# Kernel tuning notes

Hardware: AMD Instinct MI355X
Metric: run time of the kernel (lower is better)

## Reference

```python
import jax, jax.numpy as jnp
import numpy as np

B, S, D = 1024, 48, 256   # graphs, nodes-per-graph, embedding dim (= input_dim)
GDIM = 512                # graph_dim
N = B * S                 # total nodes
E = 4 * N                 # directed edges (avg degree ~4, molecular graphs)
W_SCALE = 0.05


def setup_inputs() -> dict:
    key = jax.random.key(0)
    ks = jax.random.split(key, 8)
    return {
        "sub2gene_out": jax.random.normal(ks[0], (B, S, D), jnp.float32),
        "edge_index": jax.random.randint(ks[1], (2, E), 0, N, dtype=jnp.int64),
        # conv1: in_channels = 2*D (concat of x and laplacian-smoothed x)
        "W_l1": jax.random.normal(ks[2], (GDIM, 2 * D), jnp.float32) * W_SCALE,
        "W_r1": jax.random.normal(ks[3], (GDIM, 2 * D), jnp.float32) * W_SCALE,
        "b1": jnp.zeros((GDIM,), jnp.float32),
        # conv2: graph_dim -> graph_dim
        "W_l2": jax.random.normal(ks[4], (GDIM, GDIM), jnp.float32) * W_SCALE,
        "W_r2": jax.random.normal(ks[5], (GDIM, GDIM), jnp.float32) * W_SCALE,
        "b2": jnp.zeros((GDIM,), jnp.float32),
    }


def sage_conv(x, src, dst, W_l, W_r, b, n):
    """PyG SAGEConv (mean aggregation, root_weight=True):
    out_i = W_l @ mean_{j in N(i)} x_j + W_r @ x_i + b, messages flow src->dst."""
    msg = x[src]                                            # [E, F] gather
    agg = jax.ops.segment_sum(msg, dst, num_segments=n)     # [N, F]
    cnt = jax.ops.segment_sum(jnp.ones((src.shape[0],), x.dtype), dst, num_segments=n)
    mean = agg / jnp.maximum(cnt, 1.0)[:, None]
    return mean @ W_l.T + x @ W_r.T + b


def reference(sub2gene_out, edge_index, W_l1, W_r1, b1, W_l2, W_r2, b2):
    b_, s_, d_ = sub2gene_out.shape
    n = b_ * s_
    x = sub2gene_out.reshape(n, d_)                         # cat of per-graph node features
    row, col = edge_index[0], edge_index[1]

    # sym-normalized Laplacian L = I - D^{-1/2} A D^{-1/2}; lap_x = L @ x
    ones_e = jnp.ones((row.shape[0],), x.dtype)
    deg = jax.ops.segment_sum(ones_e, row, num_segments=n)
    dinv = jnp.where(deg > 0, 1.0, 0.0) / jnp.sqrt(jnp.maximum(deg, 1.0))
    w = -(dinv[row] * dinv[col])                            # off-diagonal -A_norm
    lap_x = x + jax.ops.segment_sum(w[:, None] * x[col], row, num_segments=n)

    x_comb = jnp.concatenate([x, lap_x], axis=-1)           # [N, 2D]
    h = jax.nn.gelu(sage_conv(x_comb, row, col, W_l1, W_r1, b1, n), approximate=False)
    h = sage_conv(h, row, col, W_l2, W_r2, b2, n)           # [N, GDIM]

    # global_mean_pool: every graph has exactly s_ nodes
    batch = jnp.repeat(jnp.arange(b_), s_)
    pooled = jax.ops.segment_sum(h, batch, num_segments=b_) / jnp.asarray(s_, h.dtype)
    return pooled                                           # [B, GDIM]
```

## Files before the change

kernel.cpp:

```cpp
#include <hip/hip_runtime.h>
#include <math.h>

typedef unsigned short u16;
typedef __attribute__((ext_vector_type(8))) short bf16x8;
typedef __attribute__((ext_vector_type(4))) float f32x4;

#define NB 1024
#define NS 48
#define ND 256
#define NN (NB*NS)
#define NE (4*NN)
#define GD 512
#define KK 1024

__device__ __forceinline__ void gld16(const void* g, void* l) {
  __builtin_amdgcn_global_load_lds(
      (const __attribute__((address_space(1))) void*)(void*)g,
      (__attribute__((address_space(3))) void*)l, 16, 0, 0);
}

__device__ __forceinline__ float bf2f(u16 h) {
  unsigned u = ((unsigned)h) << 16; float f; __builtin_memcpy(&f, &u, 4); return f;
}
__device__ __forceinline__ u16 f2bf(float f) {
  unsigned u; __builtin_memcpy(&u, &f, 4);
  u += 0x7fffu + ((u >> 16) & 1u);
  return (u16)(u >> 16);
}
__device__ __forceinline__ void unpack8(uint4 v, float* f) {
  f[0]=bf2f((u16)(v.x & 0xffff)); f[1]=bf2f((u16)(v.x >> 16));
  f[2]=bf2f((u16)(v.y & 0xffff)); f[3]=bf2f((u16)(v.y >> 16));
  f[4]=bf2f((u16)(v.z & 0xffff)); f[5]=bf2f((u16)(v.z >> 16));
  f[6]=bf2f((u16)(v.w & 0xffff)); f[7]=bf2f((u16)(v.w >> 16));
}
__device__ __forceinline__ uint4 pack8(const float* f) {
  uint4 v;
  v.x = (unsigned)f2bf(f[0]) | ((unsigned)f2bf(f[1]) << 16);
  v.y = (unsigned)f2bf(f[2]) | ((unsigned)f2bf(f[3]) << 16);
  v.z = (unsigned)f2bf(f[4]) | ((unsigned)f2bf(f[5]) << 16);
  v.w = (unsigned)f2bf(f[6]) | ((unsigned)f2bf(f[7]) << 16);
  return v;
}


__global__ void k_hist(const int* __restrict__ ei, int* __restrict__ deg, int* __restrict__ cnt) {
  int e = blockIdx.x * 256 + threadIdx.x;
  if (e < NE) {
    atomicAdd(&deg[ei[e]], 1);
    atomicAdd(&cnt[ei[NE + e]], 1);
  }
}

__global__ void k_exscan2(const int* __restrict__ deg, const int* __restrict__ cnt,
                          int* __restrict__ rowOff, int* __restrict__ colOff,
                          float* __restrict__ dinv) {
  const int t = threadIdx.x;
  const int base = t * 48;
  if (blockIdx.x == 2) {
    for (int i = 0; i < 48; ++i) {
      int d = deg[base + i];
      dinv[base + i] = (d > 0) ? rsqrtf((float)d) : 0.0f;
    }
    return;
  }
  __shared__ int sums[1024];
  const int* in = blockIdx.x ? cnt : deg;
  int* out = blockIdx.x ? colOff : rowOff;
  int s = 0;
  for (int i = 0; i < 48; ++i) s += in[base + i];
  sums[t] = s;
  __syncthreads();
  for (int off = 1; off < 1024; off <<= 1) {
    int v = (t >= off) ? sums[t - off] : 0;
    __syncthreads();
    sums[t] += v;
    __syncthreads();
  }
  int run = (t == 0) ? 0 : sums[t - 1];
  for (int i = 0; i < 48; ++i) { int v = in[base + i]; out[base + i] = run; run += v; }
  if (t == 1023) out[NN] = run;
}

__global__ void k_fill(const int* __restrict__ ei,
                       const int* __restrict__ rowOff, const int* __restrict__ colOff,
                       int* __restrict__ rowFill, int* __restrict__ colFill,
                       int* __restrict__ rowCol, int* __restrict__ colSrc) {
  int e = blockIdx.x * 256 + threadIdx.x;
  if (e < NE) {
    int r = ei[e], c = ei[NE + e];
    int pr = atomicAdd(&rowFill[r], 1);
    rowCol[rowOff[r] + pr] = c;
    int pc = atomicAdd(&colFill[c], 1);
    colSrc[colOff[c] + pc] = r;
  }
}

__global__ void k_wx(const float* __restrict__ Wr1, const float* __restrict__ Wl1,
                     const float* __restrict__ Wr2, const float* __restrict__ Wl2,
                     u16* __restrict__ W1c, u16* __restrict__ W2c,
                     const float* __restrict__ x, u16* __restrict__ xb) {
  const int b = blockIdx.x;
  if (b < 1024) {
    const float* Wr = (b < 512) ? Wr1 : Wr2;
    const float* Wl = (b < 512) ? Wl1 : Wl2;
    u16* Wc = (b < 512) ? W1c : W2c;
    int i = ((b & 511) * 256 + threadIdx.x) * 4;
    int n = i >> 10, k = i & 1023;
    const float* src = (k < 512) ? (Wr + n * 512 + k) : (Wl + n * 512 + (k - 512));
    float4 v = *(const float4*)src;
    ushort4 h; h.x = f2bf(v.x); h.y = f2bf(v.y); h.z = f2bf(v.z); h.w = f2bf(v.w);
    *(ushort4*)(Wc + i) = h;
  } else {
    int i = ((b - 1024) * 256 + threadIdx.x) * 8;
    float4 v0 = *(const float4*)(x + i);
    float4 v1 = *(const float4*)(x + i + 4);
    float f[8] = {v0.x, v0.y, v0.z, v0.w, v1.x, v1.y, v1.z, v1.w};
    *(uint4*)(xb + i) = pack8(f);
  }
}

__global__ void k_lap(const u16* __restrict__ xb, const int* __restrict__ rowOff,
                      const int* __restrict__ rowCol, const float* __restrict__ dinv,
                      u16* __restrict__ xcomb) {
  const int gid = blockIdx.x * 256 + threadIdx.x;
  const int wid = gid >> 6, lane = gid & 63;
  const int node = wid * 2 + (lane >> 5);
  const int f0 = (lane & 31) * 8;
  float xi[8]; unpack8(*(const uint4*)(xb + (size_t)node * ND + f0), xi);
  float a[8] = {};
  const int s0 = rowOff[node], s1 = rowOff[node + 1];
  for (int p = s0; p < s1; p += 4) {
    const int q1 = (p + 1 < s1) ? p + 1 : s1 - 1;
    const int q2 = (p + 2 < s1) ? p + 2 : s1 - 1;
    const int q3 = (p + 3 < s1) ? p + 3 : s1 - 1;
    const int c0 = rowCol[p], c1 = rowCol[q1], c2 = rowCol[q2], c3 = rowCol[q3];
    const float w0 = dinv[c0];
    const float w1 = (p + 1 < s1) ? dinv[c1] : 0.f;
    const float w2 = (p + 2 < s1) ? dinv[c2] : 0.f;
    const float w3 = (p + 3 < s1) ? dinv[c3] : 0.f;
    float g0[8], g1[8], g2[8], g3[8];
    unpack8(*(const uint4*)(xb + (size_t)c0 * ND + f0), g0);
    unpack8(*(const uint4*)(xb + (size_t)c1 * ND + f0), g1);
    unpack8(*(const uint4*)(xb + (size_t)c2 * ND + f0), g2);
    unpack8(*(const uint4*)(xb + (size_t)c3 * ND + f0), g3);
    #pragma unroll
    for (int j = 0; j < 8; ++j) a[j] += w0 * g0[j] + w1 * g1[j] + w2 * g2[j] + w3 * g3[j];
  }
  const float di = dinv[node];
  u16* dst = xcomb + (size_t)node * KK + f0;
  *(uint4*)dst = pack8(xi);
  float l[8];
  #pragma unroll
  for (int j = 0; j < 8; ++j) l[j] = xi[j] - di * a[j];
  *(uint4*)(dst + ND) = pack8(l);
}

__global__ void k_aggx(u16* __restrict__ xcomb, const int* __restrict__ colOff,
                       const int* __restrict__ colSrc) {
  const int gid = blockIdx.x * 256 + threadIdx.x;
  const int node = gid >> 6, lane = gid & 63;
  const int f0 = lane * 8;
  float acc[8] = {};
  const int s0 = colOff[node], s1 = colOff[node + 1];
  for (int p = s0; p < s1; p += 4) {
    const int q1 = (p + 1 < s1) ? p + 1 : s1 - 1;
    const int q2 = (p + 2 < s1) ? p + 2 : s1 - 1;
    const int q3 = (p + 3 < s1) ? p + 3 : s1 - 1;
    const int c0 = colSrc[p], c1 = colSrc[q1], c2 = colSrc[q2], c3 = colSrc[q3];
    const float w1 = (p + 1 < s1) ? 1.f : 0.f;
    const float w2 = (p + 2 < s1) ? 1.f : 0.f;
    const float w3 = (p + 3 < s1) ? 1.f : 0.f;
    float g0[8], g1[8], g2[8], g3[8];
    unpack8(*(const uint4*)(xcomb + (size_t)c0 * KK + f0), g0);
    unpack8(*(const uint4*)(xcomb + (size_t)c1 * KK + f0), g1);
    unpack8(*(const uint4*)(xcomb + (size_t)c2 * KK + f0), g2);
    unpack8(*(const uint4*)(xcomb + (size_t)c3 * KK + f0), g3);
    #pragma unroll
    for (int j = 0; j < 8; ++j) acc[j] += g0[j] + w1 * g1[j] + w2 * g2[j] + w3 * g3[j];
  }
  const float inv = (s1 > s0) ? 1.0f / (float)(s1 - s0) : 1.0f;
  float res[8];
  #pragma unroll
  for (int j = 0; j < 8; ++j) res[j] = acc[j] * inv;
  *(uint4*)(xcomb + (size_t)node * KK + 512 + f0) = pack8(res);
}

template <int MODE>
__global__ __launch_bounds__(256) void k_gemm(const u16* __restrict__ A,
                                              const u16* __restrict__ Bw,
                                              const float* __restrict__ bias,
                                              void* __restrict__ OutP) {
  __shared__ u16 As[2][128 * 32];
  __shared__ u16 Bs[2][128 * 32];
  const int tid = threadIdx.x;
  const int w = tid >> 6, lane = tid & 63;
  const int wr = w >> 1, wc = w & 1;

  const int cpx = gridDim.x >> 3;
  const int o = blockIdx.x;
  const int swz = (o & 7) * cpx + (o >> 3);
  const int bx = swz >> 2;
  const int by = swz & 3;

  const int c0 = w * 2, c1 = c0 + 1;
  const int lrow = lane >> 2;
  const int lcol = ((lane & 3) ^ ((lane >> 3) & 3)) * 8;
  const u16* Ag0 = A  + (size_t)(bx * 128 + c0 * 16 + lrow) * KK + lcol;
  const u16* Ag1 = A  + (size_t)(bx * 128 + c1 * 16 + lrow) * KK + lcol;
  const u16* Bg0 = Bw + (size_t)(by * 128 + c0 * 16 + lrow) * KK + lcol;
  const u16* Bg1 = Bw + (size_t)(by * 128 + c1 * 16 + lrow) * KK + lcol;

  const int kslot = ((lane >> 4) ^ ((lane >> 1) & 3)) * 8;
  const int aoff = (wr * 64 + (lane & 15)) * 32 + kslot;
  const int boff = (wc * 64 + (lane & 15)) * 32 + kslot;

  f32x4 acc[4][4] = {};

  #define STAGE(B, KT) do {                                                \
    gld16(Ag0 + (KT), As[B] + c0 * 512);                                   \
    gld16(Ag1 + (KT), As[B] + c1 * 512);                                   \
    gld16(Bg0 + (KT), Bs[B] + c0 * 512);                                   \
    gld16(Bg1 + (KT), Bs[B] + c1 * 512);                                   \
  } while (0)

  #define COMPUTE(B) do {                                                  \
    bf16x8 aF[4], bF[4];                                                   \
    _Pragma("unroll")                                                      \
    for (int i = 0; i < 4; ++i) aF[i] = *(const bf16x8*)(As[B] + aoff + i * 512); \
    _Pragma("unroll")                                                      \
    for (int i = 0; i < 4; ++i) bF[i] = *(const bf16x8*)(Bs[B] + boff + i * 512); \
    _Pragma("unroll")                                                      \
    for (int mi = 0; mi < 4; ++mi)                                         \
      _Pragma("unroll")                                                    \
      for (int ni = 0; ni < 4; ++ni)                                       \
        acc[mi][ni] = __builtin_amdgcn_mfma_f32_16x16x32_bf16(aF[mi], bF[ni], acc[mi][ni], 0, 0, 0); \
  } while (0)

  STAGE(0, 0);
  for (int t = 0; t < 15; ++t) {
    const int k = t * 64;
    STAGE(1, k + 32);
    asm volatile("s_waitcnt vmcnt(4)" ::: "memory");
    __builtin_amdgcn_s_barrier();
    COMPUTE(0);
    __builtin_amdgcn_s_barrier();
    STAGE(0, k + 64);
    asm volatile("s_waitcnt vmcnt(4)" ::: "memory");
    __builtin_amdgcn_s_barrier();
    COMPUTE(1);
    __builtin_amdgcn_s_barrier();
  }
  STAGE(1, 992);
  asm volatile("s_waitcnt vmcnt(4)" ::: "memory");
  __builtin_amdgcn_s_barrier();
  COMPUTE(0);
  asm volatile("s_waitcnt vmcnt(0)" ::: "memory");
  __builtin_amdgcn_s_barrier();
  COMPUTE(1);
  #undef STAGE
  #undef COMPUTE

  const int lc = lane & 15, lr = (lane >> 4) * 4;
  const size_t r0 = (size_t)bx * 128 + wr * 64;
  const int cb = by * 128 + wc * 64;
  float bv[4];
  #pragma unroll
  for (int ni = 0; ni < 4; ++ni) bv[ni] = bias[cb + ni * 16 + lc];
  #pragma unroll
  for (int mi = 0; mi < 4; ++mi)
    #pragma unroll
    for (int ni = 0; ni < 4; ++ni)
      #pragma unroll
      for (int r = 0; r < 4; ++r) {
        float v = acc[mi][ni][r] + bv[ni];
        const size_t idx = (r0 + mi * 16 + lr + r) * GD + (cb + ni * 16 + lc);
        if (MODE == 0) {
          v = 0.5f * v * (1.0f + erff(v * 0.70710678118654752f));
          ((u16*)OutP)[idx] = f2bf(v);
        } else {
          ((float*)OutP)[idx] = v;
        }
      }
}

__global__ __launch_bounds__(256) void k_aggh(const u16* __restrict__ h, const int* __restrict__ colOff,
                                              const int* __restrict__ colSrc,
                                              u16* __restrict__ h2cat) {
  __shared__ float red[2][4][GD];
  const int g = blockIdx.x;
  const int t = threadIdx.x, w = t >> 6, lane = t & 63;
  const int f0 = lane * 8;
  float pr[8] = {}, pa[8] = {};
  for (int n = w; n < NS; n += 4) {
    const int node = g * NS + n;
    float tmp[8];
    unpack8(*(const uint4*)(h + (size_t)node * GD + f0), tmp);
    #pragma unroll
    for (int j = 0; j < 8; ++j) pr[j] += tmp[j];
    float acc[8] = {};
    const int s0 = colOff[node], s1 = colOff[node + 1];
    for (int p = s0; p < s1; p += 4) {
      const int q1 = (p + 1 < s1) ? p + 1 : s1 - 1;
      const int q2 = (p + 2 < s1) ? p + 2 : s1 - 1;
      const int q3 = (p + 3 < s1) ? p + 3 : s1 - 1;
      const int c0 = colSrc[p], c1 = colSrc[q1], c2 = colSrc[q2], c3 = colSrc[q3];
      const float w1 = (p + 1 < s1) ? 1.f : 0.f;
      const float w2 = (p + 2 < s1) ? 1.f : 0.f;
      const float w3 = (p + 3 < s1) ? 1.f : 0.f;
      float g0[8], g1[8], g2[8], g3[8];
      unpack8(*(const uint4*)(h + (size_t)c0 * GD + f0), g0);
      unpack8(*(const uint4*)(h + (size_t)c1 * GD + f0), g1);
      unpack8(*(const uint4*)(h + (size_t)c2 * GD + f0), g2);
      unpack8(*(const uint4*)(h + (size_t)c3 * GD + f0), g3);
      #pragma unroll
      for (int j = 0; j < 8; ++j) acc[j] += g0[j] + w1 * g1[j] + w2 * g2[j] + w3 * g3[j];
    }
    const float inv = (s1 > s0) ? 1.0f / (float)(s1 - s0) : 1.0f;
    #pragma unroll
    for (int j = 0; j < 8; ++j) pa[j] += acc[j] * inv;
  }
  #pragma unroll
  for (int j = 0; j < 8; ++j) { red[0][w][f0 + j] = pr[j]; red[1][w][f0 + j] = pa[j]; }
  __syncthreads();
  const int f = t * 2;
  const float invS = 1.0f / (float)NS;
  float r0 = (red[0][0][f] + red[0][1][f] + red[0][2][f] + red[0][3][f]) * invS;
  float r1 = (red[0][0][f+1] + red[0][1][f+1] + red[0][2][f+1] + red[0][3][f+1]) * invS;
  float a0 = (red[1][0][f] + red[1][1][f] + red[1][2][f] + red[1][3][f]) * invS;
  float a1 = (red[1][0][f+1] + red[1][1][f+1] + red[1][2][f+1] + red[1][3][f+1]) * invS;
  *(unsigned*)(h2cat + (size_t)g * KK + f)       = (unsigned)f2bf(r0) | ((unsigned)f2bf(r1) << 16);
  *(unsigned*)(h2cat + (size_t)g * KK + 512 + f) = (unsigned)f2bf(a0) | ((unsigned)f2bf(a1) << 16);
}

extern "C" void kernel_launch(void* const* d_in, const int* in_sizes, int n_in,
                              void* d_out, int out_size, void* d_ws, size_t ws_size,
                              hipStream_t stream) {
  const float* x   = (const float*)d_in[0];
  const int*   ei  = (const int*)d_in[1];
  const float* Wl1 = (const float*)d_in[2];
  const float* Wr1 = (const float*)d_in[3];
  const float* b1  = (const float*)d_in[4];
  const float* Wl2 = (const float*)d_in[5];
  const float* Wr2 = (const float*)d_in[6];
  const float* b2  = (const float*)d_in[7];
  float* out = (float*)d_out;
  (void)in_sizes; (void)n_in; (void)out_size; (void)ws_size;

  int* deg     = (int*)d_ws;
  int* cnt     = deg + NN;
  int* rowFill = cnt + NN;
  int* colFill = rowFill + NN;
  int* rowOff  = colFill + NN;
  int* colOff  = rowOff + NN + 64;
  float* dinv  = (float*)(colOff + NN + 64);
  int* rowCol  = (int*)(dinv + NN);
  int* colSrc  = rowCol + NE;
  u16* W1c     = (u16*)(colSrc + NE);
  u16* W2c     = W1c + 512 * KK;
  u16* h2cat   = W2c + 512 * KK;
  u16* xcomb   = h2cat + (size_t)NB * KK;
  u16* h       = xcomb + (size_t)NN * KK;
  u16* xb      = h;

  hipMemsetAsync(deg, 0, sizeof(int) * 4 * NN, stream);

  k_hist<<<NE / 256, 256, 0, stream>>>(ei, deg, cnt);
  k_exscan2<<<3, 1024, 0, stream>>>(deg, cnt, rowOff, colOff, dinv);
  k_fill<<<NE / 256, 256, 0, stream>>>(ei, rowOff, colOff, rowFill, colFill, rowCol, colSrc);
  k_wx<<<1024 + (NN * ND) / (256 * 8), 256, 0, stream>>>(Wr1, Wl1, Wr2, Wl2, W1c, W2c, x, xb);
  k_lap<<<(NN * 32) / 256, 256, 0, stream>>>(xb, rowOff, rowCol, dinv, xcomb);
  k_aggx<<<(NN * 64) / 256, 256, 0, stream>>>(xcomb, colOff, colSrc);

  k_gemm<0><<<(NN / 128) * 4, 256, 0, stream>>>(xcomb, W1c, b1, (void*)h);

  k_aggh<<<NB, 256, 0, stream>>>(h, colOff, colSrc, h2cat);

  k_gemm<1><<<(NB / 128) * 4, 256, 0, stream>>>(h2cat, W2c, b2, (void*)out);
}
```

Before: 283.3 us.

## Process two nodes per wave in gathers and single-buffer GEMM with BK=64

The neighbor-aggregation kernels (k_aggx, k_aggh) now have each wave handle two nodes at once, issuing eight independent row gathers per iteration to raise memory-level parallelism. The layer GEMM drops the double-buffered BK=32 pipeline for a single-buffered BK=64 tile with an XOR swizzle. It also adds a launch-bounds occupancy hint of 4 blocks per SM. The simpler GEMM loop gives up load/compute overlap inside a block in exchange for fewer barriers and more resident blocks to hide latency. Register pressure in the gather kernels rises.

```diff
diff --git a/kernel.cpp b/kernel.cpp
--- a/kernel.cpp
+++ b/kernel.cpp
@@ -158,40 +158,57 @@
 __global__ void k_aggx(u16* __restrict__ xcomb, const int* __restrict__ colOff,
                        const int* __restrict__ colSrc) {
   const int gid = blockIdx.x * 256 + threadIdx.x;
-  const int node = gid >> 6, lane = gid & 63;
+  const int wid = gid >> 6, lane = gid & 63;
+  const int n0 = wid * 2, n1 = n0 + 1;
   const int f0 = lane * 8;
-  float acc[8] = {};
-  const int s0 = colOff[node], s1 = colOff[node + 1];
-  for (int p = s0; p < s1; p += 4) {
-    const int q1 = (p + 1 < s1) ? p + 1 : s1 - 1;
-    const int q2 = (p + 2 < s1) ? p + 2 : s1 - 1;
-    const int q3 = (p + 3 < s1) ? p + 3 : s1 - 1;
-    const int c0 = colSrc[p], c1 = colSrc[q1], c2 = colSrc[q2], c3 = colSrc[q3];
-    const float w1 = (p + 1 < s1) ? 1.f : 0.f;
-    const float w2 = (p + 2 < s1) ? 1.f : 0.f;
-    const float w3 = (p + 3 < s1) ? 1.f : 0.f;
-    float g0[8], g1[8], g2[8], g3[8];
-    unpack8(*(const uint4*)(xcomb + (size_t)c0 * KK + f0), g0);
-    unpack8(*(const uint4*)(xcomb + (size_t)c1 * KK + f0), g1);
-    unpack8(*(const uint4*)(xcomb + (size_t)c2 * KK + f0), g2);
-    unpack8(*(const uint4*)(xcomb + (size_t)c3 * KK + f0), g3);
-    #pragma unroll
-    for (int j = 0; j < 8; ++j) acc[j] += g0[j] + w1 * g1[j] + w2 * g2[j] + w3 * g3[j];
-  }
-  const float inv = (s1 > s0) ? 1.0f / (float)(s1 - s0) : 1.0f;
-  float res[8];
-  #pragma unroll
-  for (int j = 0; j < 8; ++j) res[j] = acc[j] * inv;
-  *(uint4*)(xcomb + (size_t)node * KK + 512 + f0) = pack8(res);
+  const int sA = colOff[n0], sB = colOff[n0 + 1], eB = colOff[n1 + 1];
+  const int dA = sB - sA, dB = eB - sB;
+  float accA[8] = {}, accB[8] = {};
+  const int T = (dA > dB) ? dA : dB;
+  for (int t = 0; t < T; t += 4) {
+    int cA[4], cB[4];
+    float wA[4], wB[4];
+    #pragma unroll
+    for (int i = 0; i < 4; ++i) {
+      const int o = t + i;
+      int vA = colSrc[sA + ((o < dA) ? o : 0)];
+      cA[i] = (o < dA) ? vA : 0;  wA[i] = (o < dA) ? 1.f : 0.f;
+      int vB = colSrc[sB + ((o < dB) ? o : 0)];
+      cB[i] = (o < dB) ? vB : 0;  wB[i] = (o < dB) ? 1.f : 0.f;
+    }
+    uint4 gA[4], gB[4];
+    #pragma unroll
+    for (int i = 0; i < 4; ++i) {
+      gA[i] = *(const uint4*)(xcomb + (size_t)cA[i] * KK + f0);
+      gB[i] = *(const uint4*)(xcomb + (size_t)cB[i] * KK + f0);
+    }
+    #pragma unroll
+    for (int i = 0; i < 4; ++i) {
+      float tmp[8];
+      unpack8(gA[i], tmp);
+      #pragma unroll
+      for (int j = 0; j < 8; ++j) accA[j] += wA[i] * tmp[j];
+      unpack8(gB[i], tmp);
+      #pragma unroll
+      for (int j = 0; j < 8; ++j) accB[j] += wB[i] * tmp[j];
+    }
+  }
+  const float invA = (dA > 0) ? 1.0f / (float)dA : 1.0f;
+  const float invB = (dB > 0) ? 1.0f / (float)dB : 1.0f;
+  float rA[8], rB[8];
+  #pragma unroll
+  for (int j = 0; j < 8; ++j) { rA[j] = accA[j] * invA; rB[j] = accB[j] * invB; }
+  *(uint4*)(xcomb + (size_t)n0 * KK + 512 + f0) = pack8(rA);
+  *(uint4*)(xcomb + (size_t)n1 * KK + 512 + f0) = pack8(rB);
 }
 
 template <int MODE>
-__global__ __launch_bounds__(256) void k_gemm(const u16* __restrict__ A,
-                                              const u16* __restrict__ Bw,
-                                              const float* __restrict__ bias,
-                                              void* __restrict__ OutP) {
-  __shared__ u16 As[2][128 * 32];
-  __shared__ u16 Bs[2][128 * 32];
+__global__ __launch_bounds__(256, 4) void k_gemm(const u16* __restrict__ A,
+                                                 const u16* __restrict__ Bw,
+                                                 const float* __restrict__ bias,
+                                                 void* __restrict__ OutP) {
+  __shared__ u16 As[128 * 64];
+  __shared__ u16 Bs[128 * 64];
   const int tid = threadIdx.x;
   const int w = tid >> 6, lane = tid & 63;
   const int wr = w >> 1, wc = w & 1;
@@ -202,63 +219,42 @@
   const int bx = swz >> 2;
   const int by = swz & 3;
 
-  const int c0 = w * 2, c1 = c0 + 1;
-  const int lrow = lane >> 2;
-  const int lcol = ((lane & 3) ^ ((lane >> 3) & 3)) * 8;
-  const u16* Ag0 = A  + (size_t)(bx * 128 + c0 * 16 + lrow) * KK + lcol;
-  const u16* Ag1 = A  + (size_t)(bx * 128 + c1 * 16 + lrow) * KK + lcol;
-  const u16* Bg0 = Bw + (size_t)(by * 128 + c0 * 16 + lrow) * KK + lcol;
-  const u16* Bg1 = Bw + (size_t)(by * 128 + c1 * 16 + lrow) * KK + lcol;
-
-  const int kslot = ((lane >> 4) ^ ((lane >> 1) & 3)) * 8;
-  const int aoff = (wr * 64 + (lane & 15)) * 32 + kslot;
-  const int boff = (wc * 64 + (lane & 15)) * 32 + kslot;
+  const int lrow = lane >> 3;
+  const int lcol = ((lane & 7) ^ lrow) * 8;
+  const u16* Ag = A  + (size_t)(bx * 128 + w * 32 + lrow) * KK + lcol;
+  const u16* Bg = Bw + (size_t)(by * 128 + w * 32 + lrow) * KK + lcol;
+  u16* Asl = As + w * 32 * 64;
+  u16* Bsl = Bs + w * 32 * 64;
+
+  const int kg = lane >> 4;
+  const int aoff = (wr * 64 + (lane & 15)) * 64 + ((kg ^ (lane & 7)) * 8);
+  const int boff = (wc * 64 + (lane & 15)) * 64 + ((kg ^ (lane & 7)) * 8);
 
   f32x4 acc[4][4] = {};
 
-  #define STAGE(B, KT) do {                                                \
-    gld16(Ag0 + (KT), As[B] + c0 * 512);                                   \
-    gld16(Ag1 + (KT), As[B] + c1 * 512);                                   \
-    gld16(Bg0 + (KT), Bs[B] + c0 * 512);                                   \
-    gld16(Bg1 + (KT), Bs[B] + c1 * 512);                                   \
-  } while (0)
-
-  #define COMPUTE(B) do {                                                  \
-    bf16x8 aF[4], bF[4];                                                   \
-    _Pragma("unroll")                                                      \
-    for (int i = 0; i < 4; ++i) aF[i] = *(const bf16x8*)(As[B] + aoff + i * 512); \
-    _Pragma("unroll")                                                      \
-    for (int i = 0; i < 4; ++i) bF[i] = *(const bf16x8*)(Bs[B] + boff + i * 512); \
-    _Pragma("unroll")                                                      \
-    for (int mi = 0; mi < 4; ++mi)                                         \
-      _Pragma("unroll")                                                    \
-      for (int ni = 0; ni < 4; ++ni)                                       \
-        acc[mi][ni] = __builtin_amdgcn_mfma_f32_16x16x32_bf16(aF[mi], bF[ni], acc[mi][ni], 0, 0, 0); \
-  } while (0)
-
-  STAGE(0, 0);
-  for (int t = 0; t < 15; ++t) {
-    const int k = t * 64;
-    STAGE(1, k + 32);
-    asm volatile("s_waitcnt vmcnt(4)" ::: "memory");
-    __builtin_amdgcn_s_barrier();
-    COMPUTE(0);
-    __builtin_amdgcn_s_barrier();
-    STAGE(0, k + 64);
-    asm volatile("s_waitcnt vmcnt(4)" ::: "memory");
-    __builtin_amdgcn_s_barrier();
-    COMPUTE(1);
-    __builtin_amdgcn_s_barrier();
-  }
-  STAGE(1, 992);
-  asm volatile("s_waitcnt vmcnt(4)" ::: "memory");
-  __builtin_amdgcn_s_barrier();
-  COMPUTE(0);
-  asm volatile("s_waitcnt vmcnt(0)" ::: "memory");
-  __builtin_amdgcn_s_barrier();
-  COMPUTE(1);
-  #undef STAGE
-  #undef COMPUTE
+  for (int kt = 0; kt < KK; kt += 64) {
+    #pragma unroll
+    for (int c = 0; c < 4; ++c) {
+      gld16(Ag + kt + c * 8 * KK, Asl + c * 8 * 64);
+      gld16(Bg + kt + c * 8 * KK, Bsl + c * 8 * 64);
+    }
+    __syncthreads();
+    #pragma unroll
+    for (int s2 = 0; s2 < 2; ++s2) {
+      const int flip = s2 * 32;
+      bf16x8 aF[4], bF[4];
+      #pragma unroll
+      for (int i = 0; i < 4; ++i) aF[i] = *(const bf16x8*)(As + ((aoff + i * 1024) ^ flip));
+      #pragma unroll
+      for (int i = 0; i < 4; ++i) bF[i] = *(const bf16x8*)(Bs + ((boff + i * 1024) ^ flip));
+      #pragma unroll
+      for (int mi = 0; mi < 4; ++mi)
+        #pragma unroll
+        for (int ni = 0; ni < 4; ++ni)
+          acc[mi][ni] = __builtin_amdgcn_mfma_f32_16x16x32_bf16(aF[mi], bF[ni], acc[mi][ni], 0, 0, 0);
+    }
+    __syncthreads();
+  }
 
   const int lc = lane & 15, lr = (lane >> 4) * 4;
   const size_t r0 = (size_t)bx * 128 + wr * 64;
@@ -291,33 +287,53 @@
   const int t = threadIdx.x, w = t >> 6, lane = t & 63;
   const int f0 = lane * 8;
   float pr[8] = {}, pa[8] = {};
-  for (int n = w; n < NS; n += 4) {
-    const int node = g * NS + n;
+  for (int n = w; n < NS; n += 8) {
+    const int node0 = g * NS + n, node1 = node0 + 4;
     float tmp[8];
-    unpack8(*(const uint4*)(h + (size_t)node * GD + f0), tmp);
+    unpack8(*(const uint4*)(h + (size_t)node0 * GD + f0), tmp);
     #pragma unroll
     for (int j = 0; j < 8; ++j) pr[j] += tmp[j];
-    float acc[8] = {};
-    const int s0 = colOff[node], s1 = colOff[node + 1];
-    for (int p = s0; p < s1; p += 4) {
-      const int q1 = (p + 1 < s1) ? p + 1 : s1 - 1;
-      const int q2 = (p + 2 < s1) ? p + 2 : s1 - 1;
-      const int q3 = (p + 3 < s1) ? p + 3 : s1 - 1;
-      const int c0 = colSrc[p], c1 = colSrc[q1], c2 = colSrc[q2], c3 = colSrc[q3];
-      const float w1 = (p + 1 < s1) ? 1.f : 0.f;
-      const float w2 = (p + 2 < s1) ? 1.f : 0.f;
-      const float w3 = (p + 3 < s1) ? 1.f : 0.f;
-      float g0[8], g1[8], g2[8], g3[8];
-      unpack8(*(const uint4*)(h + (size_t)c0 * GD + f0), g0);
-      unpack8(*(const uint4*)(h + (size_t)c1 * GD + f0), g1);
-      unpack8(*(const uint4*)(h + (size_t)c2 * GD + f0), g2);
-      unpack8(*(const uint4*)(h + (size_t)c3 * GD + f0), g3);
-      #pragma unroll
-      for (int j = 0; j < 8; ++j) acc[j] += g0[j] + w1 * g1[j] + w2 * g2[j] + w3 * g3[j];
-    }
-    const float inv = (s1 > s0) ? 1.0f / (float)(s1 - s0) : 1.0f;
-    #pragma unroll
-    for (int j = 0; j < 8; ++j) pa[j] += acc[j] * inv;
+    unpack8(*(const uint4*)(h + (size_t)node1 * GD + f0), tmp);
+    #pragma unroll
+    for (int j = 0; j < 8; ++j) pr[j] += tmp[j];
+    const int sA = colOff[node0], eA = colOff[node0 + 1];
+    const int sB = colOff[node1], eB = colOff[node1 + 1];
+    const int dA = eA - sA, dB = eB - sB;
+    float accA[8] = {}, accB[8] = {};
+    const int T = (dA > dB) ? dA : dB;
+    for (int p = 0; p < T; p += 4) {
+      int cA[4], cB[4];
+      float wA[4], wB[4];
+      #pragma unroll
+      for (int i = 0; i < 4; ++i) {
+        const int oo = p + i;
+        int vA = colSrc[sA + ((oo < dA) ? oo : 0)];
+        cA[i] = (oo < dA) ? vA : 0;  wA[i] = (oo < dA) ? 1.f : 0.f;
+        int vB = colSrc[sB + ((oo < dB) ? oo : 0)];
+        cB[i] = (oo < dB) ? vB : 0;  wB[i] = (oo < dB) ? 1.f : 0.f;
+      }
+      uint4 gA[4], gB[4];
+      #pragma unroll
+      for (int i = 0; i < 4; ++i) {
+        gA[i] = *(const uint4*)(h + (size_t)cA[i] * GD + f0);
+        gB[i] = *(const uint4*)(h + (size_t)cB[i] * GD + f0);
+      }
+      #pragma unroll
+      for (int i = 0; i < 4; ++i) {
+        unpack8(gA[i], tmp);
+        #pragma unroll
+        for (int j = 0; j < 8; ++j) accA[j] += wA[i] * tmp[j];
+        unpack8(gB[i], tmp);
+        #pragma unroll
+        for (int j = 0; j < 8; ++j) accB[j] += wB[i] * tmp[j];
+      }
+    }
+    const float invA = (dA > 0) ? 1.0f / (float)dA : 1.0f;
+    const float invB = (dB > 0) ? 1.0f / (float)dB : 1.0f;
+    #pragma unroll
+    for (int j = 0; j < 8; ++j) pa[j] += accA[j] * invA;
+    #pragma unroll
+    for (int j = 0; j < 8; ++j) pa[j] += accB[j] * invB;
   }
   #pragma unroll
   for (int j = 0; j < 8; ++j) { red[0][w][f0 + j] = pr[j]; red[1][w][f0 + j] = pa[j]; }
@@ -369,7 +385,7 @@
   k_fill<<<NE / 256, 256, 0, stream>>>(ei, rowOff, colOff, rowFill, colFill, rowCol, colSrc);
   k_wx<<<1024 + (NN * ND) / (256 * 8), 256, 0, stream>>>(Wr1, Wl1, Wr2, Wl2, W1c, W2c, x, xb);
   k_lap<<<(NN * 32) / 256, 256, 0, stream>>>(xb, rowOff, rowCol, dinv, xcomb);
-  k_aggx<<<(NN * 64) / 256, 256, 0, stream>>>(xcomb, colOff, colSrc);
+  k_aggx<<<(NN * 32) / 256, 256, 0, stream>>>(xcomb, colOff, colSrc);
 
   k_gemm<0><<<(NN / 128) * 4, 256, 0, stream>>>(xcomb, W1c, b1, (void*)h);
 
```

New measurement: 254.5 us. 1.11x faster.
